# Optimization experiments

Measured on AMD Instinct MI355X. Metric: run time of the kernel, lower is better.

## Reference

```python
import jax, jax.numpy as jnp
import numpy as np

N, D_IN = 16384, 3
HID = 1024
R, K = 64, 64
NQ = 4096

def _glorot(key, fan_in, fan_out):
    lim = np.sqrt(6.0 / (fan_in + fan_out)).astype(np.float32)
    return jax.random.uniform(key, (fan_in, fan_out), jnp.float32, -lim, lim)

def setup_inputs() -> dict:
    key = jax.random.key(0)
    ks = jax.random.split(key, 12)
    return {
        "input": jax.random.normal(ks[0], (N, D_IN), jnp.float32),
        "eq_param": jax.random.uniform(ks[1], (1,), jnp.float32),
        "quad_x0": jax.random.uniform(ks[2], (NQ, D_IN), jnp.float32),
        "quad_x1": jax.random.uniform(ks[3], (NQ, D_IN), jnp.float32),
        # mlp_x: D_IN -> HID -> R*R
        "Wx1": _glorot(ks[4], D_IN, HID), "bx1": jnp.zeros((HID,), jnp.float32),
        "Wx2": _glorot(ks[5], HID, R * R), "bx2": jnp.zeros((R * R,), jnp.float32),
        # mlp_quad[0]: D_IN -> HID -> R*K
        "Wq0a": _glorot(ks[6], D_IN, HID), "bq0a": jnp.zeros((HID,), jnp.float32),
        "Wq0b": _glorot(ks[7], HID, R * K), "bq0b": jnp.zeros((R * K,), jnp.float32),
        # mlp_quad[1]: D_IN -> HID -> R*K
        "Wq1a": _glorot(ks[8], D_IN, HID), "bq1a": jnp.zeros((HID,), jnp.float32),
        "Wq1b": _glorot(ks[9], HID, R * K), "bq1b": jnp.zeros((R * K,), jnp.float32),
    }

def _mlp(x, W1, b1, W2, b2):
    return jnp.tanh(x @ W1 + b1) @ W2 + b2

def reference(input, eq_param, quad_x0, quad_x1,
              Wx1, bx1, Wx2, bx2,
              Wq0a, bq0a, Wq0b, bq0b,
              Wq1a, bq1a, Wq1b, bq1b):
    # r_func: Gaussian quadrature weights y_i = exp(-eq_param * ||q||^2), shape [n_i, 1]
    y0 = jnp.exp(-eq_param * jnp.sum(quad_x0 * quad_x0, axis=1, keepdims=True))
    y1 = jnp.exp(-eq_param * jnp.sum(quad_x1 * quad_x1, axis=1, keepdims=True))
    lhs = _mlp(input, Wx1, bx1, Wx2, bx2)                        # [N, R*R]
    q0 = (y0 * _mlp(quad_x0, Wq0a, bq0a, Wq0b, bq0b)).reshape(-1, R, K)  # [n0, R, K]
    q1 = (y1 * _mlp(quad_x1, Wq1a, bq1a, Wq1b, bq1b)).reshape(-1, R, K)  # [n1, R, K]
    # rhs[b,d] = sum_{a,c,x} q0[a,b,x] q1[c,d,x]
    #          = sum_x (sum_a q0[a,b,x]) (sum_c q1[c,d,x])
    # Algebraically identical to the original einsum('abx,cdx->abcd') -> movedim -> sum(0),
    # without materializing the O(n0*R*n1*R) tensor.
    S0 = q0.sum(axis=0)                                          # [R, K]
    S1 = q1.sum(axis=0)                                          # [R, K]
    rhs = S0 @ S1.T                                              # [R, R] (b, d)
    return lhs @ rhs.reshape(-1)                                 # [N]
```

## Files before the change

### kernel.cpp

```cpp
#include <hip/hip_runtime.h>

#define OFF_PART_U   0
#define OFF_PART_SY  262144
#define OFF_S        262400
#define OFF_RHS      270592
#define OFF_W2R      274688
#define OFF_C        275712

__device__ __forceinline__ float tanh_fast(float x) {
    float e = __builtin_amdgcn_exp2f(x * 2.885390081777927f);
    return 1.0f - 2.0f * __builtin_amdgcn_rcpf(e + 1.0f);
}

__global__ __launch_bounds__(256) void k1(
    const float* __restrict__ qx0, const float* __restrict__ qx1,
    const float* __restrict__ Wa0, const float* __restrict__ Wa1,
    const float* __restrict__ ba0, const float* __restrict__ ba1,
    const float* __restrict__ eqp, float* __restrict__ ws, int NQ)
{
    const int b = blockIdx.x, tid = threadIdx.x;
    const int s = b >> 7, chunk = b & 127;
    const int PPB = NQ / 128;
    const float* qx = s ? qx1 : qx0;
    const float* Wa = s ? Wa1 : Wa0;
    const float* ba = s ? ba1 : ba0;

    __shared__ float qL[32][3];
    __shared__ float yL[32];

    if (tid < 32) ws[OFF_S + b*32 + tid] = 0.0f;

    float eq = eqp[0];
    float my_y = 0.0f;
    if (tid < PPB) {
        int a = chunk * PPB + tid;
        float q0 = qx[a*3+0], q1 = qx[a*3+1], q2 = qx[a*3+2];
        qL[tid][0] = q0; qL[tid][1] = q1; qL[tid][2] = q2;
        my_y = __expf(-eq * (q0*q0 + q1*q1 + q2*q2));
        yL[tid] = my_y;
    }
    __syncthreads();

    float w0[4], w1[4], w2[4], bb4[4], acc[4];
    #pragma unroll
    for (int k = 0; k < 4; ++k) {
        int h = tid + 256*k;
        w0[k] = Wa[h]; w1[k] = Wa[1024+h]; w2[k] = Wa[2048+h];
        bb4[k] = ba[h]; acc[k] = 0.0f;
    }
    for (int a = 0; a < PPB; ++a) {
        float q0 = qL[a][0], q1 = qL[a][1], q2 = qL[a][2];
        float ya = yL[a];
        #pragma unroll
        for (int k = 0; k < 4; ++k) {
            float z = fmaf(q0, w0[k], fmaf(q1, w1[k], fmaf(q2, w2[k], bb4[k])));
            acc[k] = fmaf(ya, tanh_fast(z), acc[k]);
        }
    }
    #pragma unroll
    for (int k = 0; k < 4; ++k)
        ws[OFF_PART_U + b*1024 + tid + 256*k] = acc[k];

    if (tid < 32) {
        float v = my_y;
        #pragma unroll
        for (int off = 16; off > 0; off >>= 1) v += __shfl_down(v, off);
        if (tid == 0) ws[OFF_PART_SY + b] = v;
    }
}

__global__ __launch_bounds__(256) void k2(
    const float* __restrict__ Wb0, const float* __restrict__ Wb1,
    const float* __restrict__ bb0, const float* __restrict__ bb1,
    float* __restrict__ ws)
{
    const int bx = blockIdx.x, tid = threadIdx.x;
    const int s = bx >> 7, r = bx & 127;
    const int hc = r >> 2, jc = r & 3;
    const float* Wb = s ? Wb1 : Wb0;
    const float* bb = s ? bb1 : bb0;

    __shared__ float uRed[8][32];
    __shared__ float syL;

    int hl = tid & 31, pg = tid >> 5;
    float accu = 0.0f;
    #pragma unroll 4
    for (int p = pg*16; p < pg*16 + 16; ++p)
        accu += ws[OFF_PART_U + (s*128 + p)*1024 + hc*32 + hl];
    uRed[pg][hl] = accu;
    float sv = 0.0f;
    if (tid < 64)
        sv = ws[OFF_PART_SY + s*128 + tid] + ws[OFF_PART_SY + s*128 + 64 + tid];
    __syncthreads();
    if (tid < 32) {
        float t = 0.0f;
        #pragma unroll
        for (int g = 0; g < 8; ++g) t += uRed[g][tid];
        uRed[0][tid] = t;
    }
    if (tid < 64) {
        #pragma unroll
        for (int off = 32; off > 0; off >>= 1) sv += __shfl_down(sv, off);
        if (tid == 0) syL = sv;
    }
    __syncthreads();

    float sy = syL;
    int j = jc * 1024 + tid * 4;
    float4 acc;
    if (hc == 0) {
        float4 b4 = *reinterpret_cast<const float4*>(bb + j);
        acc = make_float4(sy*b4.x, sy*b4.y, sy*b4.z, sy*b4.w);
    } else {
        acc = make_float4(0.f, 0.f, 0.f, 0.f);
    }
    const float* row = Wb + (hc*32)*4096 + j;
    #pragma unroll 8
    for (int h = 0; h < 32; ++h) {
        float4 w = *reinterpret_cast<const float4*>(row);
        float uh = uRed[0][h];
        acc.x = fmaf(uh, w.x, acc.x);
        acc.y = fmaf(uh, w.y, acc.y);
        acc.z = fmaf(uh, w.z, acc.z);
        acc.w = fmaf(uh, w.w, acc.w);
        row += 4096;
    }
    float* S = ws + OFF_S + s * 4096;
    atomicAdd(&S[j+0], acc.x);
    atomicAdd(&S[j+1], acc.y);
    atomicAdd(&S[j+2], acc.z);
    atomicAdd(&S[j+3], acc.w);
}

__global__ __launch_bounds__(256) void k3(float* __restrict__ ws)
{
    __shared__ float S0L[4096];
    __shared__ float S1T[64 * 65];
    const float* S0 = ws + OFF_S;
    const float* S1 = ws + OFF_S + 4096;
    float* rhs = ws + OFF_RHS;
    int tid = threadIdx.x;
    for (int i = tid; i < 4096; i += 256) {
        S0L[i] = S0[i];
        int d = i >> 6, x = i & 63;
        S1T[x * 65 + d] = S1[i];
    }
    __syncthreads();
    int o = blockIdx.x * 256 + tid;
    int b = o >> 6, d = o & 63;
    float acc = 0.0f;
    #pragma unroll 8
    for (int x = 0; x < 64; ++x)
        acc = fmaf(S0L[b*64 + x], S1T[x*65 + d], acc);
    rhs[o] = acc;
}

__global__ __launch_bounds__(256) void k4(
    const float* __restrict__ Wx2, const float* __restrict__ bx2,
    float* __restrict__ ws)
{
    __shared__ float4 rhsL[1024];
    const float4* rhs4 = reinterpret_cast<const float4*>(ws + OFF_RHS);
    int tid = threadIdx.x;
    for (int i = tid; i < 1024; i += 256) rhsL[i] = rhs4[i];
    __syncthreads();
    int wave = tid >> 6, lane = tid & 63;
    int rowIdx = blockIdx.x * 4 + wave;
    if (rowIdx > 1024) return;
    const float4* src4 = reinterpret_cast<const float4*>(
        (rowIdx < 1024) ? (Wx2 + rowIdx * 4096) : bx2);
    float acc = 0.0f;
    #pragma unroll
    for (int i = 0; i < 16; ++i) {
        float4 w  = src4[lane + 64*i];
        float4 rv = rhsL[lane + 64*i];
        acc += w.x*rv.x + w.y*rv.y + w.z*rv.z + w.w*rv.w;
    }
    #pragma unroll
    for (int off = 32; off > 0; off >>= 1) acc += __shfl_down(acc, off);
    if (lane == 0) {
        if (rowIdx < 1024) ws[OFF_W2R + rowIdx] = acc;
        else               ws[OFF_C] = acc;
    }
}

__global__ __launch_bounds__(256) void k5(
    const float* __restrict__ input, const float* __restrict__ Wx1,
    const float* __restrict__ bx1, const float* __restrict__ ws,
    float* __restrict__ out, int N)
{
    __shared__ float4 WL[1024];
    __shared__ float w2rL[1024];
    int tid = threadIdx.x;
    #pragma unroll
    for (int k = 0; k < 4; ++k) {
        int h = tid + 256*k;
        WL[h] = make_float4(Wx1[h], Wx1[1024+h], Wx1[2048+h], bx1[h]);
        w2rL[h] = ws[OFF_W2R + h];
    }
    __syncthreads();
    float c = ws[OFF_C];
    int n = blockIdx.x * 32 + (tid >> 3);
    int p = tid & 7;
    int nc = (n < N) ? n : (N - 1);
    float in0 = input[nc*3+0], in1 = input[nc*3+1], in2 = input[nc*3+2];
    float acc = 0.0f;
    #pragma unroll 4
    for (int i = 0; i < 128; ++i) {
        int h = 8*i + p;
        float4 w = WL[h];
        float z = fmaf(in0, w.x, fmaf(in1, w.y, fmaf(in2, w.z, w.w)));
        acc = fmaf(tanh_fast(z), w2rL[h], acc);
    }
    acc += __shfl_xor(acc, 1);
    acc += __shfl_xor(acc, 2);
    acc += __shfl_xor(acc, 4);
    if (p == 0 && n < N) out[n] = acc + c;
}

extern "C" void kernel_launch(void* const* d_in, const int* in_sizes, int n_in,
                              void* d_out, int out_size, void* d_ws, size_t ws_size,
                              hipStream_t stream)
{
    const float* input = (const float*)d_in[0];
    const float* eqp   = (const float*)d_in[1];
    const float* qx0   = (const float*)d_in[2];
    const float* qx1   = (const float*)d_in[3];
    const float* Wx1   = (const float*)d_in[4];
    const float* bx1   = (const float*)d_in[5];
    const float* Wx2   = (const float*)d_in[6];
    const float* bx2   = (const float*)d_in[7];
    const float* Wq0a  = (const float*)d_in[8];
    const float* bq0a  = (const float*)d_in[9];
    const float* Wq0b  = (const float*)d_in[10];
    const float* bq0b  = (const float*)d_in[11];
    const float* Wq1a  = (const float*)d_in[12];
    const float* bq1a  = (const float*)d_in[13];
    const float* Wq1b  = (const float*)d_in[14];
    const float* bq1b  = (const float*)d_in[15];
    float* ws  = (float*)d_ws;
    float* out = (float*)d_out;

    int N  = in_sizes[0] / 3;
    int NQ = in_sizes[2] / 3;

    hipLaunchKernelGGL(k1, dim3(256), dim3(256), 0, stream,
                       qx0, qx1, Wq0a, Wq1a, bq0a, bq1a, eqp, ws, NQ);
    hipLaunchKernelGGL(k2, dim3(256), dim3(256), 0, stream,
                       Wq0b, Wq1b, bq0b, bq1b, ws);
    hipLaunchKernelGGL(k3, dim3(16), dim3(256), 0, stream, ws);
    hipLaunchKernelGGL(k4, dim3(257), dim3(256), 0, stream, Wx2, bx2, ws);
    hipLaunchKernelGGL(k5, dim3((N + 31) / 32), dim3(256), 0, stream,
                       input, Wx1, bx1, ws, out, N);
}
```

Baseline: 138.4 us.

## Fuse rhs outer-product into W2·rhs kernel and double k2 grid

Merges the small S0·S1ᵀ kernel into the W2-row dot-product kernel. Each of the 257 blocks now recomputes the full 64x64 rhs in shared memory, which removes one launch and the global round-trip for rhs. The cost is redundant compute (4096x64 FMAs per block) and about 48KB of LDS per block, which may limit occupancy. Separately, k2 is split into 512 blocks, each reducing 16 hidden units instead of 32, to add parallelism, though this doubles the atomic adds into S.

Measured after the change: 150.7 us. 8.9% more time.

```diff
diff --git a/kernel.cpp b/kernel.cpp
--- a/kernel.cpp
+++ b/kernel.cpp
@@ -3,9 +3,8 @@
 #define OFF_PART_U   0
 #define OFF_PART_SY  262144
 #define OFF_S        262400
-#define OFF_RHS      270592
-#define OFF_W2R      274688
-#define OFF_C        275712
+#define OFF_W2R      270592
+#define OFF_C        271616
 
 __device__ __forceinline__ float tanh_fast(float x) {
     float e = __builtin_amdgcn_exp2f(x * 2.885390081777927f);
@@ -75,29 +74,30 @@
     float* __restrict__ ws)
 {
     const int bx = blockIdx.x, tid = threadIdx.x;
-    const int s = bx >> 7, r = bx & 127;
+    const int s = bx >> 8, r = bx & 255;
     const int hc = r >> 2, jc = r & 3;
     const float* Wb = s ? Wb1 : Wb0;
     const float* bb = s ? bb1 : bb0;
 
-    __shared__ float uRed[8][32];
+    __shared__ float uRed[16][16];
+    __shared__ float uFin[16];
     __shared__ float syL;
 
-    int hl = tid & 31, pg = tid >> 5;
+    int hl = tid & 15, pg = tid >> 4;
     float accu = 0.0f;
-    #pragma unroll 4
-    for (int p = pg*16; p < pg*16 + 16; ++p)
-        accu += ws[OFF_PART_U + (s*128 + p)*1024 + hc*32 + hl];
+    #pragma unroll
+    for (int p = pg*8; p < pg*8 + 8; ++p)
+        accu += ws[OFF_PART_U + (s*128 + p)*1024 + hc*16 + hl];
     uRed[pg][hl] = accu;
     float sv = 0.0f;
     if (tid < 64)
         sv = ws[OFF_PART_SY + s*128 + tid] + ws[OFF_PART_SY + s*128 + 64 + tid];
     __syncthreads();
-    if (tid < 32) {
+    if (tid < 16) {
         float t = 0.0f;
         #pragma unroll
-        for (int g = 0; g < 8; ++g) t += uRed[g][tid];
-        uRed[0][tid] = t;
+        for (int g = 0; g < 16; ++g) t += uRed[g][tid];
+        uFin[tid] = t;
     }
     if (tid < 64) {
         #pragma unroll
@@ -115,11 +115,11 @@
     } else {
         acc = make_float4(0.f, 0.f, 0.f, 0.f);
     }
-    const float* row = Wb + (hc*32)*4096 + j;
+    const float* row = Wb + (hc*16)*4096 + j;
     #pragma unroll 8
-    for (int h = 0; h < 32; ++h) {
+    for (int h = 0; h < 16; ++h) {
         float4 w = *reinterpret_cast<const float4*>(row);
-        float uh = uRed[0][h];
+        float uh = uFin[h];
         acc.x = fmaf(uh, w.x, acc.x);
         acc.y = fmaf(uh, w.y, acc.y);
         acc.z = fmaf(uh, w.z, acc.z);
@@ -133,48 +133,43 @@
     atomicAdd(&S[j+3], acc.w);
 }
 
-__global__ __launch_bounds__(256) void k3(float* __restrict__ ws)
+__global__ __launch_bounds__(256) void k34(
+    const float* __restrict__ Wx2, const float* __restrict__ bx2,
+    float* __restrict__ ws)
 {
     __shared__ float S0L[4096];
     __shared__ float S1T[64 * 65];
-    const float* S0 = ws + OFF_S;
-    const float* S1 = ws + OFF_S + 4096;
-    float* rhs = ws + OFF_RHS;
-    int tid = threadIdx.x;
+    __shared__ __align__(16) float rhsL[4096];
+    const int tid = threadIdx.x;
+    const float* S = ws + OFF_S;
     for (int i = tid; i < 4096; i += 256) {
-        S0L[i] = S0[i];
+        S0L[i] = S[i];
         int d = i >> 6, x = i & 63;
-        S1T[x * 65 + d] = S1[i];
-    }
-    __syncthreads();
-    int o = blockIdx.x * 256 + tid;
-    int b = o >> 6, d = o & 63;
-    float acc = 0.0f;
-    #pragma unroll 8
-    for (int x = 0; x < 64; ++x)
-        acc = fmaf(S0L[b*64 + x], S1T[x*65 + d], acc);
-    rhs[o] = acc;
-}
-
-__global__ __launch_bounds__(256) void k4(
-    const float* __restrict__ Wx2, const float* __restrict__ bx2,
-    float* __restrict__ ws)
-{
-    __shared__ float4 rhsL[1024];
-    const float4* rhs4 = reinterpret_cast<const float4*>(ws + OFF_RHS);
-    int tid = threadIdx.x;
-    for (int i = tid; i < 1024; i += 256) rhsL[i] = rhs4[i];
+        S1T[x * 65 + d] = S[4096 + i];
+    }
+    __syncthreads();
+    #pragma unroll
+    for (int k = 0; k < 16; ++k) {
+        int o = k*256 + tid;
+        int br = o >> 6, d = o & 63;
+        float acc = 0.0f;
+        #pragma unroll 8
+        for (int x = 0; x < 64; ++x)
+            acc = fmaf(S0L[br*64 + x], S1T[x*65 + d], acc);
+        rhsL[o] = acc;
+    }
     __syncthreads();
     int wave = tid >> 6, lane = tid & 63;
     int rowIdx = blockIdx.x * 4 + wave;
     if (rowIdx > 1024) return;
     const float4* src4 = reinterpret_cast<const float4*>(
         (rowIdx < 1024) ? (Wx2 + rowIdx * 4096) : bx2);
+    const float4* rhs4 = reinterpret_cast<const float4*>(rhsL);
     float acc = 0.0f;
     #pragma unroll
     for (int i = 0; i < 16; ++i) {
         float4 w  = src4[lane + 64*i];
-        float4 rv = rhsL[lane + 64*i];
+        float4 rv = rhs4[lane + 64*i];
         acc += w.x*rv.x + w.y*rv.y + w.z*rv.z + w.w*rv.w;
     }
     #pragma unroll
@@ -247,10 +242,9 @@
 
     hipLaunchKernelGGL(k1, dim3(256), dim3(256), 0, stream,
                        qx0, qx1, Wq0a, Wq1a, bq0a, bq1a, eqp, ws, NQ);
-    hipLaunchKernelGGL(k2, dim3(256), dim3(256), 0, stream,
+    hipLaunchKernelGGL(k2, dim3(512), dim3(256), 0, stream,
                        Wq0b, Wq1b, bq0b, bq1b, ws);
-    hipLaunchKernelGGL(k3, dim3(16), dim3(256), 0, stream, ws);
-    hipLaunchKernelGGL(k4, dim3(257), dim3(256), 0, stream, Wx2, bx2, ws);
+    hipLaunchKernelGGL(k34, dim3(257), dim3(256), 0, stream, Wx2, bx2, ws);
     hipLaunchKernelGGL(k5, dim3((N + 31) / 32), dim3(256), 0, stream,
                        input, Wx1, bx1, ws, out, N);
 }
```
